# Kernel optimization log

Hardware: AMD Instinct MI355X
Metric: run time of the kernel (lower is better)

Reference implementation:

```python
import math
import jax, jax.numpy as jnp
from jax import lax
import numpy as np

B, S2, D = 8, 1024, 768  # seq_len = 32*32 spatial tokens
HD = 64                   # head_dim
K = 7                     # LocalRmsNorm kernel_size
EPS = 1e-7


def setup_inputs() -> dict:
    key = jax.random.key(0)
    ks = jax.random.split(key, 6)
    sc = 0.02
    return {
        "x": jax.random.normal(ks[0], (B, S2, D), jnp.float32),
        "norm_w": jnp.ones((D,), jnp.float32),
        "wq": jax.random.normal(ks[1], (D, D), jnp.float32) * sc,
        "bq": jnp.zeros((D,), jnp.float32),
        "wk": jax.random.normal(ks[2], (D, D), jnp.float32) * sc,
        "bk": jnp.zeros((D,), jnp.float32),
        "wv": jax.random.normal(ks[3], (D, D), jnp.float32) * sc,
        "bv": jnp.zeros((D,), jnp.float32),
        "wo": jax.random.normal(ks[4], (D, D), jnp.float32) * sc,
        "bo": jnp.zeros((D,), jnp.float32),
    }


def local_rms_norm(x, w):
    # x: [b, s*s, d]; sliding KxK box-sum of squares over the s x s grid,
    # zero-padded (matches F.unfold), mean divisor is always K*K.
    b, ss, d = x.shape
    s = int(math.isqrt(ss))
    sq = (x * x).reshape(b, s, s, d)
    box = lax.reduce_window(sq, 0.0, lax.add,
                            (1, K, K, 1), (1, 1, 1, 1), 'SAME')
    rms = jnp.sqrt(EPS + box / (K * K)).reshape(b, ss, d)
    return x / rms * w


def reference(x, norm_w, wq, bq, wk, bk, wv, bv, wo, bo):
    xn = local_rms_norm(x, norm_w)
    b, s, d = xn.shape
    h = d // HD

    def proj(w_, b_):
        return (xn @ w_.T + b_).reshape(b, s, h, HD).transpose(0, 2, 1, 3)

    q = proj(wq, bq)  # [b, h, s, dh]
    k = proj(wk, bk)
    v = proj(wv, bv)
    scores = jnp.einsum('bhqd,bhkd->bhqk', q, k) / math.sqrt(HD)
    attn = jax.nn.softmax(scores, axis=-1)
    out = jnp.einsum('bhqk,bhkd->bhqd', attn, v)
    out = out.transpose(0, 2, 1, 3).reshape(b, s, d)
    return out @ wo.T + bo
```

## Files before the change

### kernel.cpp

```cpp
#include <hip/hip_runtime.h>

typedef _Float16 f16x8 __attribute__((ext_vector_type(8)));
typedef _Float16 f16x4 __attribute__((ext_vector_type(4)));
typedef _Float16 f16x2 __attribute__((ext_vector_type(2)));
typedef float    f32x4 __attribute__((ext_vector_type(4)));
typedef float    f32x16 __attribute__((ext_vector_type(16)));
typedef unsigned int u32x4 __attribute__((ext_vector_type(4)));
typedef unsigned short ushort_t;
typedef unsigned int uint_t;

#define LOG2E 1.44269504088896340736f

#define CFENCE  asm volatile("" ::: "memory")
#define HWBAR   __builtin_amdgcn_s_barrier()
#define VMCNT0  asm volatile("s_waitcnt vmcnt(0)" ::: "memory")
#define VMCNT3  asm volatile("s_waitcnt vmcnt(3)" ::: "memory")
#define VMCNT4  asm volatile("s_waitcnt vmcnt(4)" ::: "memory")

__device__ __forceinline__ ushort_t f2h(float x) {
  _Float16 h = (_Float16)x;
  return __builtin_bit_cast(ushort_t, h);
}

__device__ __forceinline__ float fexp2(float x) {
#if __has_builtin(__builtin_amdgcn_exp2f)
  return __builtin_amdgcn_exp2f(x);
#else
  float r; asm("v_exp_f32 %0, %1" : "=v"(r) : "v"(x)); return r;
#endif
}

__device__ __forceinline__ float frsq(float x) {
#if __has_builtin(__builtin_amdgcn_rsqf)
  return __builtin_amdgcn_rsqf(x);
#else
  float r; asm("v_rsq_f32 %0, %1" : "=v"(r) : "v"(x)); return r;
#endif
}

__device__ __forceinline__ uint_t packpair(float a, float b) {
  return __builtin_bit_cast(uint_t, __builtin_amdgcn_cvt_pkrtz(a, b));
}

__device__ __forceinline__ f16x8 mk8(uint_t a, uint_t b, uint_t c, uint_t d) {
  u32x4 t; t[0] = a; t[1] = b; t[2] = c; t[3] = d;
  return __builtin_bit_cast(f16x8, t);
}

__device__ __forceinline__ void gload_lds16(const void* g, void* lds) {
  __builtin_amdgcn_global_load_lds(
      (const __attribute__((address_space(1))) void*)(uintptr_t)g,
      (__attribute__((address_space(3))) void*)(unsigned)(uintptr_t)lds,
      16, 0, 0);
}


__global__ __launch_bounds__(256)
void lrn_a(const float* __restrict__ x, ushort_t* __restrict__ tmp) {
  int tid = blockIdx.x * 256 + threadIdx.x;
  int dv  = tid % 192;
  int rem = tid / 192;
  int pos = rem & 1023;
  int b   = rem >> 10;
  int r = pos >> 5, c = pos & 31;
  const float4* base = (const float4*)x + ((size_t)b * 1024 + (size_t)r * 32) * 192 + dv;
  float ax = 0.f, ay = 0.f, az = 0.f, aw = 0.f;
#pragma unroll
  for (int dc = -3; dc <= 3; ++dc) {
    int cc = c + dc;
    if (cc >= 0 && cc < 32) {
      float4 v = base[cc * 192];
      ax += v.x * v.x; ay += v.y * v.y; az += v.z * v.z; aw += v.w * v.w;
    }
  }
  f16x4 o;
  o[0] = (_Float16)ax; o[1] = (_Float16)ay; o[2] = (_Float16)az; o[3] = (_Float16)aw;
  *(f16x4*)(tmp + (size_t)tid * 4) = o;
}

__global__ __launch_bounds__(256)
void lrn_b(const float* __restrict__ x, const ushort_t* __restrict__ tmp,
           const float* __restrict__ wn, ushort_t* __restrict__ xn) {
  int tid = blockIdx.x * 256 + threadIdx.x;
  int dv  = tid % 192;
  int rem = tid / 192;
  int pos = rem & 1023;
  int b   = rem >> 10;
  int r = pos >> 5, c = pos & 31;
  const ushort_t* tb = tmp + (((size_t)b * 1024 + c) * 192 + dv) * 4;
  float ax = 0.f, ay = 0.f, az = 0.f, aw = 0.f;
#pragma unroll
  for (int dr = -3; dr <= 3; ++dr) {
    int rr = r + dr;
    if (rr >= 0 && rr < 32) {
      f16x4 v = *(const f16x4*)(tb + (size_t)rr * 24576);
      ax += (float)v[0]; ay += (float)v[1]; az += (float)v[2]; aw += (float)v[3];
    }
  }
  float4 xv = ((const float4*)x)[tid];
  float4 wv = ((const float4*)wn)[dv];
  const float inv49 = 1.0f / 49.0f;
  float i0 = frsq(1e-7f + ax * inv49);
  float i1 = frsq(1e-7f + ay * inv49);
  float i2 = frsq(1e-7f + az * inv49);
  float i3 = frsq(1e-7f + aw * inv49);
  f16x4 o;
  o[0] = (_Float16)(xv.x * i0 * wv.x);
  o[1] = (_Float16)(xv.y * i1 * wv.y);
  o[2] = (_Float16)(xv.z * i2 * wv.z);
  o[3] = (_Float16)(xv.w * i3 * wv.w);
  const int m = b * 1024 + pos;
  const int panel = m >> 4, lrr = m & 15;
  const int kc = dv >> 3, lg2 = (dv >> 1) & 3, half = dv & 1;
  *(f16x4*)(xn + ((size_t)((panel * 24 + kc) * 64 + lg2 * 16 + lrr)) * 8 + half * 4) = o;
}

__global__ __launch_bounds__(256)
void convw_fm(const float* __restrict__ wq, const float* __restrict__ wk,
              const float* __restrict__ wv, const float* __restrict__ wo,
              ushort_t* __restrict__ bqkv, ushort_t* __restrict__ bwo) {
  const int g = blockIdx.x * 256 + threadIdx.x;
  const int mat = g / 73728;
  const int gg = g % 73728;
  const int panel = gg / 1536;
  const int rem = gg % 1536;
  const int kc = rem >> 6, l = rem & 63;
  const int row = panel * 16 + (l & 15);
  const int col = kc * 32 + (l >> 4) * 8;
  const float* src = (mat == 0) ? wq : (mat == 1) ? wk : (mat == 2) ? wv : wo;
  const float4 v0 = *(const float4*)(src + (size_t)row * 768 + col);
  const float4 v1 = *(const float4*)(src + (size_t)row * 768 + col + 4);
  f16x8 o;
  o[0]=(_Float16)v0.x; o[1]=(_Float16)v0.y; o[2]=(_Float16)v0.z; o[3]=(_Float16)v0.w;
  o[4]=(_Float16)v1.x; o[5]=(_Float16)v1.y; o[6]=(_Float16)v1.z; o[7]=(_Float16)v1.w;
  if (mat < 3) *(f16x8*)(bqkv + (size_t)g * 8) = o;
  else         *(f16x8*)(bwo  + (size_t)gg * 8) = o;
}

#define GSTAGE(BUF, KT) do {                                                      \
    _Pragma("unroll")                                                             \
    for (int j = 0; j < SI; ++j)                                                  \
      gload_lds16(sb[j] + (KT) * 512, (BUF) ? d1[j] : d0[j]);                     \
  } while (0)

#define GTILE(KT, CUR, NXT) do {                                                  \
    CFENCE; HWBAR; CFENCE;                              \
    if ((KT) + 1 < 24) {                                                          \
      GSTAGE(NXT, (KT) + 1);                                                      \
      if constexpr (SI == 4) VMCNT4; else VMCNT3;       \
    } else VMCNT0;                                                                \
    CFENCE; HWBAR;                                \
    __builtin_amdgcn_sched_barrier(0);                                            \
    f16x8 af[MT], bf[NT];                                                         \
    _Pragma("unroll")                                                             \
    for (int mt = 0; mt < MT; ++mt)                                               \
      af[mt] = *(const f16x8*)(&As[CUR][(wr * MT + mt) * 512 + l * 8]);           \
    _Pragma("unroll")                                                             \
    for (int nt = 0; nt < NT; ++nt)                                               \
      bf[nt] = *(const f16x8*)(&Bs[CUR][(wc * NT + nt) * 512 + l * 8]);           \
    _Pragma("unroll")                                                             \
    for (int mt = 0; mt < MT; ++mt)                                               \
      _Pragma("unroll")                                                           \
      for (int nt = 0; nt < NT; ++nt)                                             \
        acc[mt][nt] = __builtin_amdgcn_mfma_f32_16x16x32_f16(af[mt], bf[nt], acc[mt][nt], 0, 0, 0); \
  } while (0)

template <int MODE>
__global__ __launch_bounds__(256)
void gemm_lds(const ushort_t* __restrict__ Afm, const ushort_t* __restrict__ Bfm,
              const float* __restrict__ b0, const float* __restrict__ b1,
              const float* __restrict__ b2,
              ushort_t* __restrict__ q, ushort_t* __restrict__ k,
              ushort_t* __restrict__ v, float* __restrict__ outf) {
  constexpr int PM  = (MODE == 0) ? 8 : 4;
  constexpr int PN  = 8;
  constexpr int NBN = (MODE == 0) ? 18 : 6;
  constexpr int SI  = (PM + PN) / 4;
  constexpr int MT  = PM / 2, NT = PN / 2;
  __shared__ __align__(16) ushort_t As[2][PM * 512];
  __shared__ __align__(16) ushort_t Bs[2][PN * 512];

  const int nwg = gridDim.x;
  const int bid = blockIdx.x;
  const int cid = (bid & 7) * (nwg >> 3) + (bid >> 3);
  const int bm = cid / NBN, bn = cid % NBN;
  const int tid = threadIdx.x;
  const int w = tid >> 6, l = tid & 63;
  const int wr = w >> 1, wc = w & 1;
  const int lr = l & 15, lg = l >> 4;

  f32x4 acc[MT][NT] = {};

  const ushort_t* sb[SI];
  ushort_t* d0[SI];
  ushort_t* d1[SI];
#pragma unroll
  for (int j = 0; j < SI; ++j) {
    const int g = w * SI + j;
    if (g < PM) {
      sb[j] = Afm + ((size_t)(bm * PM + g) * 24) * 512 + l * 8;
      d0[j] = &As[0][g * 512]; d1[j] = &As[1][g * 512];
    } else {
      sb[j] = Bfm + ((size_t)(bn * PN + (g - PM)) * 24) * 512 + l * 8;
      d0[j] = &Bs[0][(g - PM) * 512]; d1[j] = &Bs[1][(g - PM) * 512];
    }
  }

  GSTAGE(0, 0);
  for (int kt = 0; kt < 24; kt += 2) {
    GTILE(kt, 0, 1);
    GTILE(kt + 1, 1, 0);
  }

#pragma unroll
  for (int mt = 0; mt < MT; ++mt) {
#pragma unroll
    for (int nt = 0; nt < NT; ++nt) {
      if (MODE == 0) {
        const int n = bn * 128 + wc * 64 + nt * 16 + lr;
        const int mbase = bm * 128 + wr * 64 + mt * 16 + lg * 4;
        const int region = n / 768;
        const int nn = n - region * 768;
        const int hh = nn >> 6, hd = nn & 63;
        const float bb = (region == 0 ? b0 : region == 1 ? b1 : b2)[nn];
        const int khalf = (hd >> 3) & 1, kch = hd >> 4, jd = hd & 7;
        if (region == 2) {
          const int bi = mbase >> 10, s0 = mbase & 1023;
          const int tile = s0 >> 6, q6 = s0 & 63;
          const int aa = q6 >> 5, r5 = q6 & 31;
          const int t1 = r5 >> 3, h2 = (r5 >> 2) & 1;
          const int gq = t1 >> 1, jj = (2 * t1) & 3;
          const int chunk = (aa << 1) + gq;
          const int gidx = (hd >> 5) * 4 + chunk;
          const int lane = (hd & 31) + 32 * h2;
          f16x4 pv;
#pragma unroll
          for (int gi = 0; gi < 4; ++gi) pv[gi] = (_Float16)(acc[mt][nt][gi] + bb);
          *(f16x4*)(v + (((size_t)(bi * 12 + hh) * 16 + tile) * 8 + gidx) * 512
                      + lane * 8 + 2 * jj) = pv;
        } else {
#pragma unroll
          for (int gi = 0; gi < 4; ++gi) {
            const int m = mbase + gi;
            const int bi = m >> 10, s = m & 1023;
            const float val = acc[mt][nt][gi] + bb;
            if (region == 0) {
              const int lane = (s & 31) + 32 * khalf;
              q[(((size_t)(bi * 12 + hh) * 32 + (s >> 5)) * 4 + kch) * 512
                + lane * 8 + jd] = f2h(val * (0.125f * LOG2E));
            } else {
              const int lane = (s & 31) + 32 * khalf;
              k[(((size_t)(bi * 12 + hh) * 16 + (s >> 6)) * 8
                 + ((s >> 5) & 1) * 4 + kch) * 512 + lane * 8 + jd] = f2h(val);
            }
          }
        }
      } else {
        const int n = bn * 128 + wc * 64 + nt * 16 + lr;
        const float bb = b0[n];
#pragma unroll
        for (int gi = 0; gi < 4; ++gi) {
          const int m = bm * 64 + wr * 32 + mt * 16 + lg * 4 + gi;
          outf[(size_t)m * 768 + n] = acc[mt][nt][gi] + bb;
        }
      }
    }
  }
}

#define ATILE(T, CUR, NXT) do {                                                   \
    CFENCE; HWBAR; CFENCE;                              \
    if ((T) < 15) {                                                               \
      const ushort_t* ksrc = kp + (size_t)((T) + 1) * 4096;                       \
      const ushort_t* vsrc = vp + (size_t)((T) + 1) * 4096;                       \
      gload_lds16(ksrc + tid * 8,           Kl0 + (NXT) * 8192);                  \
      gload_lds16(ksrc + (tid + 256) * 8,   Kl1 + (NXT) * 8192);                  \
      gload_lds16(vsrc + tid * 8,           Vl0 + (NXT) * 8192);                  \
      gload_lds16(vsrc + (tid + 256) * 8,   Vl1 + (NXT) * 8192);                  \
      VMCNT4;                                        \
    } else VMCNT0;                                                                \
    CFENCE; HWBAR;                            \
    __builtin_amdgcn_sched_barrier(0);                                            \
    const char* kbase = (const char*)smem + (CUR) * 8192;                         \
    const char* vbase = (const char*)smem + 16384 + (CUR) * 8192;                 \
    f16x8 ka0[4], ka1[4];                                                         \
    _Pragma("unroll")                                                             \
    for (int kc = 0; kc < 4; ++kc) {                                              \
      ka0[kc] = *(const f16x8*)(kbase + kc * 1024 + l * 16);                      \
      ka1[kc] = *(const f16x8*)(kbase + 4096 + kc * 1024 + l * 16);               \
    }                                                                             \
    f32x16 s0v = {}, s1v = {};                                                    \
    __builtin_amdgcn_s_setprio(1);                                                \
    _Pragma("unroll")                                                             \
    for (int kc = 0; kc < 4; ++kc) {                                              \
      s0v = __builtin_amdgcn_mfma_f32_32x32x16_f16(ka0[kc], qf[kc], s0v, 0, 0, 0);\
      s1v = __builtin_amdgcn_mfma_f32_32x32x16_f16(ka1[kc], qf[kc], s1v, 0, 0, 0);\
    }                                                                             \
    __builtin_amdgcn_s_setprio(0);                                                \
    f16x8 va0[4], va1[4];                                                         \
    _Pragma("unroll")                                                             \
    for (int c = 0; c < 4; ++c) {                                                 \
      va0[c] = *(const f16x8*)(vbase + c * 1024 + l * 16);                        \
      va1[c] = *(const f16x8*)(vbase + 4096 + c * 1024 + l * 16);                 \
    }                                                                             \
    uint_t pk0[8], pk1[8];                                                        \
    _Pragma("unroll")                                                             \
    for (int tt = 0; tt < 8; ++tt) {                                              \
      pk0[tt] = packpair(fexp2(s0v[2 * tt]), fexp2(s0v[2 * tt + 1]));             \
      pk1[tt] = packpair(fexp2(s1v[2 * tt]), fexp2(s1v[2 * tt + 1]));             \
    }                                                                             \
    _Pragma("unroll")                                                             \
    for (int tt = 0; tt < 4; ++tt) {                                              \
      lr0 = __builtin_amdgcn_fdot2(__builtin_bit_cast(f16x2, pk0[tt]),     one2, lr0, false); \
      lr1 = __builtin_amdgcn_fdot2(__builtin_bit_cast(f16x2, pk0[tt + 4]), one2, lr1, false); \
      lr2 = __builtin_amdgcn_fdot2(__builtin_bit_cast(f16x2, pk1[tt]),     one2, lr2, false); \
      lr3 = __builtin_amdgcn_fdot2(__builtin_bit_cast(f16x2, pk1[tt + 4]), one2, lr3, false); \
    }                                                                             \
    const f16x8 pb0 = mk8(pk0[0], pk0[1], pk0[2], pk0[3]);                        \
    const f16x8 pb1 = mk8(pk0[4], pk0[5], pk0[6], pk0[7]);                        \
    const f16x8 pb2 = mk8(pk1[0], pk1[1], pk1[2], pk1[3]);                        \
    const f16x8 pb3 = mk8(pk1[4], pk1[5], pk1[6], pk1[7]);                        \
    __builtin_amdgcn_s_setprio(1);                                                \
    oacc0 = __builtin_amdgcn_mfma_f32_32x32x16_f16(va0[0], pb0, oacc0, 0, 0, 0);  \
    oacc1 = __builtin_amdgcn_mfma_f32_32x32x16_f16(va1[0], pb0, oacc1, 0, 0, 0);  \
    oacc0 = __builtin_amdgcn_mfma_f32_32x32x16_f16(va0[1], pb1, oacc0, 0, 0, 0);  \
    oacc1 = __builtin_amdgcn_mfma_f32_32x32x16_f16(va1[1], pb1, oacc1, 0, 0, 0);  \
    oacc0 = __builtin_amdgcn_mfma_f32_32x32x16_f16(va0[2], pb2, oacc0, 0, 0, 0);  \
    oacc1 = __builtin_amdgcn_mfma_f32_32x32x16_f16(va1[2], pb2, oacc1, 0, 0, 0);  \
    oacc0 = __builtin_amdgcn_mfma_f32_32x32x16_f16(va0[3], pb3, oacc0, 0, 0, 0);  \
    oacc1 = __builtin_amdgcn_mfma_f32_32x32x16_f16(va1[3], pb3, oacc1, 0, 0, 0);  \
    __builtin_amdgcn_s_setprio(0);                                                \
  } while (0)

__global__ __launch_bounds__(256, 3)
void attn_fused11(const ushort_t* __restrict__ qb, const ushort_t* __restrict__ kb,
                  const ushort_t* __restrict__ vt, ushort_t* __restrict__ ao) {
  __shared__ __align__(16) ushort_t smem[16384];
  const int tid = threadIdx.x;
  const int w = tid >> 6, l = tid & 63;
  const int lq = l & 31, hi = l >> 5;

  const int bid = blockIdx.x;
  const int cid = (bid & 7) * 96 + (bid >> 3);
  const int bh = cid >> 3, qt = cid & 7;
  const int b = bh / 12, h = bh % 12;

  const ushort_t* qp = qb + ((size_t)(bh * 32 + qt * 4 + w)) * 2048;
  const ushort_t* kp = kb + (size_t)bh * 65536;
  const ushort_t* vp = vt + (size_t)bh * 65536;

  f16x8 qf[4];
#pragma unroll
  for (int kc = 0; kc < 4; ++kc)
    qf[kc] = *(const f16x8*)(qp + kc * 512 + l * 8);

  char* Kl0 = (char*)smem + w * 1024;
  char* Kl1 = (char*)smem + 4096 + w * 1024;
  char* Vl0 = (char*)smem + 16384 + w * 1024;
  char* Vl1 = (char*)smem + 16384 + 4096 + w * 1024;

  f32x16 oacc0 = {}, oacc1 = {};
  float lr0 = 0.f, lr1 = 0.f, lr2 = 0.f, lr3 = 0.f;
  const f16x2 one2 = {(_Float16)1.f, (_Float16)1.f};

  gload_lds16(kp + tid * 8,         Kl0);
  gload_lds16(kp + (tid + 256) * 8, Kl1);
  gload_lds16(vp + tid * 8,         Vl0);
  gload_lds16(vp + (tid + 256) * 8, Vl1);

  for (int t2 = 0; t2 < 16; t2 += 2) {
    ATILE(t2, 0, 1);
    ATILE(t2 + 1, 1, 0);
  }

  float lrun = (lr0 + lr1) + (lr2 + lr3);
  lrun += __shfl_xor(lrun, 32, 64);
  const float invl = 1.0f / lrun;

  __syncthreads();

  uint_t* ot = (uint_t*)smem + w * 1024 + lq * 32;
#pragma unroll
  for (int tt = 0; tt < 8; ++tt) {
    const int base = (tt & 1) + ((tt >> 1) << 2) + 2 * hi;
    ot[base ^ lq]        = packpair(oacc0[2 * tt] * invl, oacc0[2 * tt + 1] * invl);
    ot[(base + 16) ^ lq] = packpair(oacc1[2 * tt] * invl, oacc1[2 * tt + 1] * invl);
  }
  __syncthreads();
  const int row = tid >> 1, halfc = tid & 1;
  const int w2 = row >> 5, qq = row & 31;
  const uint_t* srcp = (const uint_t*)smem + w2 * 1024 + qq * 32;
  const int m = b * 1024 + qt * 128 + row;
  const int panel = m >> 4, lrr = m & 15;
  const int kc = h * 2 + halfc;
#pragma unroll
  for (int jj = 0; jj < 4; ++jj) {
    u32x4 tv;
#pragma unroll
    for (int i2 = 0; i2 < 4; ++i2)
      tv[i2] = srcp[(halfc * 16 + jj * 4 + i2) ^ qq];
    *(u32x4*)(ao + ((size_t)((panel * 24 + kc) * 64 + jj * 16 + lrr)) * 8) = tv;
  }
}

extern "C" void kernel_launch(void* const* d_in, const int* in_sizes, int n_in,
                              void* d_out, int out_size, void* d_ws, size_t ws_size,
                              hipStream_t stream) {
  const float* x  = (const float*)d_in[0];
  const float* nw = (const float*)d_in[1];
  const float* wq = (const float*)d_in[2];
  const float* bq = (const float*)d_in[3];
  const float* wk = (const float*)d_in[4];
  const float* bk = (const float*)d_in[5];
  const float* wv = (const float*)d_in[6];
  const float* bv = (const float*)d_in[7];
  const float* wo = (const float*)d_in[8];
  const float* bo = (const float*)d_in[9];
  float* out = (float*)d_out;

  char* ws = (char*)d_ws;
  ushort_t* tmp   = (ushort_t*)ws;
  ushort_t* qbuf  = (ushort_t*)(ws);
  ushort_t* kbuf  = (ushort_t*)(ws + 12582912);
  ushort_t* xnf   = (ushort_t*)(ws + 25165824);
  ushort_t* bwqkv = (ushort_t*)(ws + 37748736);
  ushort_t* bwo   = (ushort_t*)(ws + 41287680);
  ushort_t* vtb   = (ushort_t*)(ws + 42467328);
  ushort_t* aoutf = (ushort_t*)(ws + 55050240);

  lrn_a<<<6144, 256, 0, stream>>>(x, tmp);
  lrn_b<<<6144, 256, 0, stream>>>(x, tmp, nw, xnf);
  convw_fm<<<1152, 256, 0, stream>>>(wq, wk, wv, wo, bwqkv, bwo);
  gemm_lds<0><<<1152, 256, 0, stream>>>(xnf, bwqkv, bq, bk, bv,
                                        qbuf, kbuf, vtb, nullptr);
  attn_fused11<<<768, 256, 0, stream>>>(qbuf, kbuf, vtb, aoutf);
  gemm_lds<1><<<768, 256, 0, stream>>>(aoutf, bwo, bo, nullptr, nullptr,
                                       nullptr, nullptr, nullptr, out);
}
```

Before: 135.6 us.

## Widen QKV GEMM tile to 128x256 with 8 waves per block

The QKV projection GEMM now uses 512-thread blocks with 8 waves arranged 2x4, covering a 128x256 output tile instead of 128x128, and the grid is halved to 576 blocks. Each A panel loaded into LDS is reused across twice as many output columns, which cuts global and LDS staging traffic per FLOP. The vmcnt wait is unified to 3, since each thread now issues 3 staging loads in both modes. The cost is a larger LDS footprint per block, fewer blocks to spread across CUs, and possible occupancy or tail effects. The attention kernel's shared buffer is renamed with no functional change.

```diff
diff --git a/kernel.cpp b/kernel.cpp
--- a/kernel.cpp
+++ b/kernel.cpp
@@ -147,7 +147,7 @@
     CFENCE; HWBAR; CFENCE;                              \
     if ((KT) + 1 < 24) {                                                          \
       GSTAGE(NXT, (KT) + 1);                                                      \
-      if constexpr (SI == 4) VMCNT4; else VMCNT3;       \
+      VMCNT3;                                           \
     } else VMCNT0;                                                                \
     CFENCE; HWBAR;                                \
     __builtin_amdgcn_sched_barrier(0);                                            \
@@ -166,17 +166,19 @@
   } while (0)
 
 template <int MODE>
-__global__ __launch_bounds__(256)
+__global__ __launch_bounds__(MODE == 0 ? 512 : 256)
 void gemm_lds(const ushort_t* __restrict__ Afm, const ushort_t* __restrict__ Bfm,
               const float* __restrict__ b0, const float* __restrict__ b1,
               const float* __restrict__ b2,
               ushort_t* __restrict__ q, ushort_t* __restrict__ k,
               ushort_t* __restrict__ v, float* __restrict__ outf) {
+  constexpr int NW  = (MODE == 0) ? 8 : 4;
   constexpr int PM  = (MODE == 0) ? 8 : 4;
-  constexpr int PN  = 8;
-  constexpr int NBN = (MODE == 0) ? 18 : 6;
-  constexpr int SI  = (PM + PN) / 4;
-  constexpr int MT  = PM / 2, NT = PN / 2;
+  constexpr int PN  = (MODE == 0) ? 16 : 8;
+  constexpr int NBN = (MODE == 0) ? 9 : 6;
+  constexpr int SI  = (PM + PN) / NW;
+  constexpr int MT  = PM / 2;
+  constexpr int NT  = 4;
   __shared__ __align__(16) ushort_t As[2][PM * 512];
   __shared__ __align__(16) ushort_t Bs[2][PN * 512];
 
@@ -186,7 +188,8 @@
   const int bm = cid / NBN, bn = cid % NBN;
   const int tid = threadIdx.x;
   const int w = tid >> 6, l = tid & 63;
-  const int wr = w >> 1, wc = w & 1;
+  const int wr = (MODE == 0) ? (w >> 2) : (w >> 1);
+  const int wc = (MODE == 0) ? (w & 3) : (w & 1);
   const int lr = l & 15, lg = l >> 4;
 
   f32x4 acc[MT][NT] = {};
@@ -212,12 +215,13 @@
     GTILE(kt + 1, 1, 0);
   }
 
+  constexpr int BNW = (MODE == 0) ? 256 : 128;
 #pragma unroll
   for (int mt = 0; mt < MT; ++mt) {
 #pragma unroll
     for (int nt = 0; nt < NT; ++nt) {
       if (MODE == 0) {
-        const int n = bn * 128 + wc * 64 + nt * 16 + lr;
+        const int n = bn * BNW + wc * 64 + nt * 16 + lr;
         const int mbase = bm * 128 + wr * 64 + mt * 16 + lg * 4;
         const int region = n / 768;
         const int nn = n - region * 768;
@@ -256,7 +260,7 @@
           }
         }
       } else {
-        const int n = bn * 128 + wc * 64 + nt * 16 + lr;
+        const int n = bn * BNW + wc * 64 + nt * 16 + lr;
         const float bb = b0[n];
 #pragma unroll
         for (int gi = 0; gi < 4; ++gi) {
@@ -281,8 +285,8 @@
     } else VMCNT0;                                                                \
     CFENCE; HWBAR;                            \
     __builtin_amdgcn_sched_barrier(0);                                            \
-    const char* kbase = (const char*)smem + (CUR) * 8192;                         \
-    const char* vbase = (const char*)smem + 16384 + (CUR) * 8192;                 \
+    const char* kbase = (const char*)asmem + (CUR) * 8192;                        \
+    const char* vbase = (const char*)asmem + 16384 + (CUR) * 8192;                \
     f16x8 ka0[4], ka1[4];                                                         \
     _Pragma("unroll")                                                             \
     for (int kc = 0; kc < 4; ++kc) {                                              \
@@ -335,7 +339,7 @@
 __global__ __launch_bounds__(256, 3)
 void attn_fused11(const ushort_t* __restrict__ qb, const ushort_t* __restrict__ kb,
                   const ushort_t* __restrict__ vt, ushort_t* __restrict__ ao) {
-  __shared__ __align__(16) ushort_t smem[16384];
+  __shared__ __align__(16) ushort_t asmem[16384];
   const int tid = threadIdx.x;
   const int w = tid >> 6, l = tid & 63;
   const int lq = l & 31, hi = l >> 5;
@@ -354,10 +358,10 @@
   for (int kc = 0; kc < 4; ++kc)
     qf[kc] = *(const f16x8*)(qp + kc * 512 + l * 8);
 
-  char* Kl0 = (char*)smem + w * 1024;
-  char* Kl1 = (char*)smem + 4096 + w * 1024;
-  char* Vl0 = (char*)smem + 16384 + w * 1024;
-  char* Vl1 = (char*)smem + 16384 + 4096 + w * 1024;
+  char* Kl0 = (char*)asmem + w * 1024;
+  char* Kl1 = (char*)asmem + 4096 + w * 1024;
+  char* Vl0 = (char*)asmem + 16384 + w * 1024;
+  char* Vl1 = (char*)asmem + 16384 + 4096 + w * 1024;
 
   f32x16 oacc0 = {}, oacc1 = {};
   float lr0 = 0.f, lr1 = 0.f, lr2 = 0.f, lr3 = 0.f;
@@ -379,7 +383,7 @@
 
   __syncthreads();
 
-  uint_t* ot = (uint_t*)smem + w * 1024 + lq * 32;
+  uint_t* ot = (uint_t*)asmem + w * 1024 + lq * 32;
 #pragma unroll
   for (int tt = 0; tt < 8; ++tt) {
     const int base = (tt & 1) + ((tt >> 1) << 2) + 2 * hi;
@@ -389,7 +393,7 @@
   __syncthreads();
   const int row = tid >> 1, halfc = tid & 1;
   const int w2 = row >> 5, qq = row & 31;
-  const uint_t* srcp = (const uint_t*)smem + w2 * 1024 + qq * 32;
+  const uint_t* srcp = (const uint_t*)asmem + w2 * 1024 + qq * 32;
   const int m = b * 1024 + qt * 128 + row;
   const int panel = m >> 4, lrr = m & 15;
   const int kc = h * 2 + halfc;
@@ -431,8 +435,8 @@
   lrn_a<<<6144, 256, 0, stream>>>(x, tmp);
   lrn_b<<<6144, 256, 0, stream>>>(x, tmp, nw, xnf);
   convw_fm<<<1152, 256, 0, stream>>>(wq, wk, wv, wo, bwqkv, bwo);
-  gemm_lds<0><<<1152, 256, 0, stream>>>(xnf, bwqkv, bq, bk, bv,
-                                        qbuf, kbuf, vtb, nullptr);
+  gemm_lds<0><<<576, 512, 0, stream>>>(xnf, bwqkv, bq, bk, bv,
+                                       qbuf, kbuf, vtb, nullptr);
   attn_fused11<<<768, 256, 0, stream>>>(qbuf, kbuf, vtb, aoutf);
   gemm_lds<1><<<768, 256, 0, stream>>>(aoutf, bwo, bo, nullptr, nullptr,
                                        nullptr, nullptr, nullptr, out);
```

After: 134.7 us. Within noise of the previous version (-0.7%).
